# Optimization experiments

Hardware: AMD Instinct MI355X
Metric: run time of the kernel (lower is better)

The kernel has to match this reference:

```python
import jax, jax.numpy as jnp
import numpy as np

D_MODEL = 1024
NUM_HEADS = 16
D_K = D_MODEL // NUM_HEADS


def setup_inputs() -> dict:
    key = jax.random.key(0)
    ks = jax.random.split(key, 11)
    B, S = 2, 2048
    s = 1.0 / np.sqrt(D_MODEL)
    return {
        "query": jax.random.normal(ks[0], (B, S, D_MODEL), jnp.float32),
        "key": jax.random.normal(ks[1], (B, S, D_MODEL), jnp.float32),
        "value": jax.random.normal(ks[2], (B, S, D_MODEL), jnp.float32),
        "Wq": jax.random.normal(ks[3], (D_MODEL, D_MODEL), jnp.float32) * s,
        "bq": jnp.zeros((D_MODEL,), jnp.float32),
        "Wk": jax.random.normal(ks[4], (D_MODEL, D_MODEL), jnp.float32) * s,
        "bk": jnp.zeros((D_MODEL,), jnp.float32),
        "Wv": jax.random.normal(ks[5], (D_MODEL, D_MODEL), jnp.float32) * s,
        "bv": jnp.zeros((D_MODEL,), jnp.float32),
        "Wo": jax.random.normal(ks[6], (D_MODEL, D_MODEL), jnp.float32) * s,
        "bo": jnp.zeros((D_MODEL,), jnp.float32),
    }


def _split_heads(x):
    # [B, S, D] -> [B, H, S, d_k]
    B, S, _ = x.shape
    return x.reshape(B, S, NUM_HEADS, D_K).transpose(0, 2, 1, 3)


def reference(query, key, value, Wq, bq, Wk, bk, Wv, bv, Wo, bo):
    B, S, _ = query.shape
    q = _split_heads(query @ Wq + bq)   # [B, H, S, d_k]
    k = _split_heads(key @ Wk + bk)
    v = _split_heads(value @ Wv + bv)
    scores = jnp.einsum("bhqd,bhkd->bhqk", q, k) / jnp.sqrt(jnp.float32(D_K))
    attention_weights = jax.nn.softmax(scores, axis=-1)  # [B, H, S, S]
    context = jnp.einsum("bhqk,bhkd->bhqd", attention_weights, v)
    context = context.transpose(0, 2, 1, 3).reshape(B, S, D_MODEL)
    output = context @ Wo + bo
    return (output, attention_weights)
```

## Files before the change

kernel.cpp:

```cpp
#include <hip/hip_runtime.h>
#include <hip/hip_bf16.h>


#define SEQ   2048
#define DMODEL 1024
#define NH    16
#define DKH   64

typedef __attribute__((ext_vector_type(8))) short  short8;
typedef __attribute__((ext_vector_type(4))) float  floatx4;

__device__ __forceinline__ short f2bf(float f) {
    __hip_bfloat16 h = __float2bfloat16(f);
    return *reinterpret_cast<short*>(&h);
}
__device__ __forceinline__ unsigned int packbf(float a, float b) {
    return (unsigned int)(unsigned short)f2bf(a) | ((unsigned int)(unsigned short)f2bf(b) << 16);
}

__device__ __forceinline__ void gload_lds16(const short* g, short* l) {
    __builtin_amdgcn_global_load_lds(
        (const __attribute__((address_space(1))) void*)g,
        (__attribute__((address_space(3))) void*)l, 16, 0, 0);
}

__global__ void conv3(const float* __restrict__ s0, const float* __restrict__ s1,
                      const float* __restrict__ s2, short* __restrict__ d0,
                      short* __restrict__ d1, short* __restrict__ d2) {
    int z = blockIdx.z;
    const float* src = z == 0 ? s0 : z == 1 ? s1 : s2;
    short* dst       = z == 0 ? d0 : z == 1 ? d1 : d2;
    int i = blockIdx.x * blockDim.x + threadIdx.x;
    float4 v = reinterpret_cast<const float4*>(src)[i];
    short4 o;
    o.x = f2bf(v.x); o.y = f2bf(v.y); o.z = f2bf(v.z); o.w = f2bf(v.w);
    reinterpret_cast<short4*>(dst)[i] = o;
}

__global__ void conv_wt4(const float* __restrict__ W0, const float* __restrict__ W1,
                         const float* __restrict__ W2, const float* __restrict__ W3,
                         short* __restrict__ T0, short* __restrict__ T1,
                         short* __restrict__ T2, short* __restrict__ T3) {
    __shared__ short T[64 * 72];
    int z = blockIdx.z;
    const float* W = z == 0 ? W0 : z == 1 ? W1 : z == 2 ? W2 : W3;
    short* Wt      = z == 0 ? T0 : z == 1 ? T1 : z == 2 ? T2 : T3;
    int tid = threadIdx.x;
    int bk = blockIdx.y, bn = blockIdx.x;
    for (int i = 0; i < 4; i++) {
        int ch = i * 256 + tid;
        int r = ch >> 4, c4 = (ch & 15) * 4;
        float4 v = *(const float4*)&W[(size_t)(bk * 64 + r) * 1024 + bn * 64 + c4];
        T[(c4 + 0) * 72 + r] = f2bf(v.x);
        T[(c4 + 1) * 72 + r] = f2bf(v.y);
        T[(c4 + 2) * 72 + r] = f2bf(v.z);
        T[(c4 + 3) * 72 + r] = f2bf(v.w);
    }
    __syncthreads();
    for (int i = 0; i < 2; i++) {
        int ch = i * 256 + tid;
        int n = ch >> 3, k8 = (ch & 7) * 8;
        *(short8*)&Wt[(size_t)(bn * 64 + n) * 1024 + bk * 64 + k8] = *(const short8*)&T[n * 72 + k8];
    }
}

__device__ __forceinline__ void gemm_body(
    const short* __restrict__ A, const short* __restrict__ Bt,
    const float* __restrict__ bias, void* __restrict__ dst, int mode)
{
    __shared__ __align__(16) short As[2][128 * 32];
    __shared__ __align__(16) short Bs[2][64 * 32];
    int tid = threadIdx.x;
    int wave = tid >> 6, lane = tid & 63, quad = lane >> 4, l15 = lane & 15;
    int bm = blockIdx.y, bn = blockIdx.x;

    floatx4 acc[2][4];
#pragma unroll
    for (int i = 0; i < 2; i++)
#pragma unroll
        for (int j = 0; j < 4; j++) acc[i][j] = (floatx4){0.f, 0.f, 0.f, 0.f};

    const short* aBase = &A [(size_t)(bm * 128 + (tid >> 2)) * 1024 + (tid & 3) * 8];
    const short* bBase = &Bt[(size_t)(bn * 64  + (tid >> 2)) * 1024 + (tid & 3) * 8];

#define STAGE(buf, kb) do {                                              \
        gload_lds16(aBase + (kb) * 32,             &As[buf][(wave * 64) * 8]);         \
        gload_lds16(aBase + 64 * 1024 + (kb) * 32, &As[buf][(256 + wave * 64) * 8]);   \
        gload_lds16(bBase + (kb) * 32,             &Bs[buf][(wave * 64) * 8]);         \
    } while (0)

    STAGE(0, 0);
    __syncthreads();
    int cur = 0;
    for (int kb = 0; kb < 32; kb++) {
        if (kb < 31) STAGE(cur ^ 1, kb + 1);
        short8 ar[2], br[4];
#pragma unroll
        for (int mt = 0; mt < 2; mt++) ar[mt] = *(const short8*)&As[cur][(wave * 32 + mt * 16 + l15) * 32 + quad * 8];
#pragma unroll
        for (int nt = 0; nt < 4; nt++) br[nt] = *(const short8*)&Bs[cur][(nt * 16 + l15) * 32 + quad * 8];
#pragma unroll
        for (int mt = 0; mt < 2; mt++)
#pragma unroll
            for (int nt = 0; nt < 4; nt++)
                acc[mt][nt] = __builtin_amdgcn_mfma_f32_16x16x32_bf16(ar[mt], br[nt], acc[mt][nt], 0, 0, 0);
        __syncthreads();
        cur ^= 1;
    }
#undef STAGE

#pragma unroll
    for (int mt = 0; mt < 2; mt++) {
#pragma unroll
        for (int nt = 0; nt < 4; nt++) {
            int col = bn * 64 + nt * 16 + l15;
            float bb = bias[col];
#pragma unroll
            for (int r = 0; r < 4; r++) {
                int row = bm * 128 + wave * 32 + mt * 16 + quad * 4 + r;
                float v = acc[mt][nt][r] + bb;
                if (mode == 3) {
                    ((float*)dst)[(size_t)row * 1024 + col] = v;
                } else {
                    int b = row >> 11, s = row & 2047, h = col >> 6, dk = col & 63;
                    size_t idx;
                    if (mode == 0) idx = ((size_t)(b * NH + h) * SEQ + s) * DKH + dk;
                    else           idx = ((size_t)(b * NH + h) * DKH + dk) * SEQ + s;
                    ((short*)dst)[idx] = f2bf(v);
                }
            }
        }
    }
}

__global__ __launch_bounds__(256, 4) void gemm_qkv(
    const short* __restrict__ xq, const short* __restrict__ xk, const short* __restrict__ xv,
    const short* __restrict__ wq, const short* __restrict__ wk, const short* __restrict__ wv,
    const float* __restrict__ bq, const float* __restrict__ bk, const float* __restrict__ bv,
    short* __restrict__ qh, short* __restrict__ kh, short* __restrict__ vth)
{
    int z = blockIdx.z;
    const short* A  = z == 0 ? xq : z == 1 ? xk : xv;
    const short* Bt = z == 0 ? wq : z == 1 ? wk : wv;
    const float* bi = z == 0 ? bq : z == 1 ? bk : bv;
    short* dst      = z == 0 ? qh : z == 1 ? kh : vth;
    gemm_body(A, Bt, bi, dst, z == 2 ? 2 : 0);
}

__global__ __launch_bounds__(256, 4) void gemm_fin(
    const short* __restrict__ A, const short* __restrict__ Bt,
    const float* __restrict__ bias, float* __restrict__ dst)
{
    gemm_body(A, Bt, bias, dst, 3);
}

__global__ __launch_bounds__(256, 2) void attn_p1(
    const short* __restrict__ Q,
    const short* __restrict__ K,
    const short* __restrict__ Vt,
    float* __restrict__ rws,
    short* __restrict__ ctx)
{
    __shared__ __align__(16) short Qs [64 * 72];
    __shared__ __align__(16) short Ks [128 * 72];
    __shared__ __align__(16) short Vts[64 * 136];
    __shared__ __align__(16) short Ps [64 * 136];
    __shared__ float partial[4][64];
    __shared__ float rinv[64];

    int tid = threadIdx.x, wave = tid >> 6, lane = tid & 63, quad = lane >> 4, l15 = lane & 15;
    int qt = blockIdx.x, bh = blockIdx.y;
    int b = bh >> 4, h = bh & 15;
    const short* qb  = Q  + ((size_t)bh * SEQ + qt * 64) * DKH;
    const short* kbp = K  + (size_t)bh * SEQ * DKH;
    const short* vtb = Vt + (size_t)bh * DKH * SEQ;

#pragma unroll
    for (int c = 0; c < 2; c++) {
        int ch = tid * 2 + c; int row = ch >> 3, d = (ch & 7) * 8;
        *(short8*)&Qs[row * 72 + d] = *(const short8*)&qb[row * 64 + d];
    }

    short8 kreg[4], vreg[4];
#define LOADKV(kb) do {                                                              \
        _Pragma("unroll")                                                            \
        for (int c = 0; c < 4; c++) { int ch = tid * 4 + c; int row = ch >> 3, d = (ch & 7) * 8; \
            kreg[c] = *(const short8*)&kbp[(size_t)((kb) * 128 + row) * 64 + d]; }   \
        _Pragma("unroll")                                                            \
        for (int c = 0; c < 4; c++) { int ch = tid * 4 + c; int dd = ch >> 4, kq = (ch & 15) * 8; \
            vreg[c] = *(const short8*)&vtb[(size_t)dd * SEQ + (kb) * 128 + kq]; }    \
    } while (0)

    LOADKV(0);

    float rs[4][4];
#pragma unroll
    for (int i = 0; i < 4; i++)
#pragma unroll
        for (int r = 0; r < 4; r++) rs[i][r] = 0.f;
    floatx4 cacc[4];
#pragma unroll
    for (int i = 0; i < 4; i++) cacc[i] = (floatx4){0.f, 0.f, 0.f, 0.f};
    int nbase = wave * 32;

    for (int kb = 0; kb < SEQ / 128; kb++) {
        __syncthreads();
#pragma unroll
        for (int c = 0; c < 4; c++) {
            int ch = tid * 4 + c; int row = ch >> 3, d = (ch & 7) * 8;
            *(short8*)&Ks[row * 72 + d] = kreg[c];
        }
#pragma unroll
        for (int c = 0; c < 4; c++) {
            int ch = tid * 4 + c; int dd = ch >> 4, kq = (ch & 15) * 8;
            *(short8*)&Vts[dd * 136 + kq] = vreg[c];
        }
        __syncthreads();
        if (kb < SEQ / 128 - 1) LOADKV(kb + 1);

        floatx4 sacc[4][2];
#pragma unroll
        for (int mt = 0; mt < 4; mt++)
#pragma unroll
            for (int nt = 0; nt < 2; nt++) sacc[mt][nt] = (floatx4){0.f, 0.f, 0.f, 0.f};
#pragma unroll
        for (int kt = 0; kt < 2; kt++) {
            short8 ar[4], br[2];
#pragma unroll
            for (int mt = 0; mt < 4; mt++) ar[mt] = *(const short8*)&Qs[(mt * 16 + l15) * 72 + kt * 32 + quad * 8];
#pragma unroll
            for (int nt = 0; nt < 2; nt++) br[nt] = *(const short8*)&Ks[(nbase + 2 * l15 + nt) * 72 + kt * 32 + quad * 8];
#pragma unroll
            for (int mt = 0; mt < 4; mt++)
#pragma unroll
                for (int nt = 0; nt < 2; nt++)
                    sacc[mt][nt] = __builtin_amdgcn_mfma_f32_16x16x32_bf16(ar[mt], br[nt], sacc[mt][nt], 0, 0, 0);
        }
#pragma unroll
        for (int mt = 0; mt < 4; mt++) {
#pragma unroll
            for (int r = 0; r < 4; r++) {
                float e0 = __expf(sacc[mt][0][r] * 0.125f);
                float e1 = __expf(sacc[mt][1][r] * 0.125f);
                int row = mt * 16 + quad * 4 + r;
                *(unsigned int*)&Ps[row * 136 + nbase + 2 * l15] = packbf(e0, e1);
                rs[mt][r] += e0 + e1;
            }
        }
        __syncthreads();
#pragma unroll
        for (int kt = 0; kt < 4; kt++) {
            short8 pa = *(const short8*)&Ps[(wave * 16 + l15) * 136 + kt * 32 + quad * 8];
#pragma unroll
            for (int nt = 0; nt < 4; nt++) {
                short8 vb = *(const short8*)&Vts[(nt * 16 + l15) * 136 + kt * 32 + quad * 8];
                cacc[nt] = __builtin_amdgcn_mfma_f32_16x16x32_bf16(pa, vb, cacc[nt], 0, 0, 0);
            }
        }
    }
#undef LOADKV

#pragma unroll
    for (int mt = 0; mt < 4; mt++) {
#pragma unroll
        for (int r = 0; r < 4; r++) {
            float s = rs[mt][r];
            s += __shfl_xor(s, 1, 64); s += __shfl_xor(s, 2, 64);
            s += __shfl_xor(s, 4, 64); s += __shfl_xor(s, 8, 64);
            if (l15 == 0) partial[wave][mt * 16 + quad * 4 + r] = s;
        }
    }
    __syncthreads();
    if (tid < 64) {
        float ri = 1.f / (partial[0][tid] + partial[1][tid] + partial[2][tid] + partial[3][tid]);
        rinv[tid] = ri;
        rws[((size_t)bh * 32 + qt) * 64 + tid] = ri;
    }
    __syncthreads();

#pragma unroll
    for (int nt = 0; nt < 4; nt++) {
#pragma unroll
        for (int r = 0; r < 4; r++) {
            int row = wave * 16 + quad * 4 + r;
            int qg = qt * 64 + row;
            float v = cacc[nt][r] * rinv[row];
            ctx[((size_t)(b * SEQ + qg)) * DMODEL + h * DKH + nt * 16 + l15] = f2bf(v);
        }
    }
}

__global__ __launch_bounds__(256, 4) void attn_p2(
    const short* __restrict__ Q, const short* __restrict__ K,
    const float* __restrict__ rws, float* __restrict__ wout)
{
    __shared__ __align__(16) short Qs[64 * 72];
    __shared__ __align__(16) short Ks[128 * 72];
    __shared__ float rinv[64];

    int tid = threadIdx.x, wave = tid >> 6, lane = tid & 63, quad = lane >> 4, l15 = lane & 15;
    int qt = blockIdx.x, bh = blockIdx.y;
    const short* qb  = Q + ((size_t)bh * SEQ + qt * 64) * DKH;
    const short* kbp = K + (size_t)bh * SEQ * DKH;

#pragma unroll
    for (int c = 0; c < 2; c++) {
        int ch = tid * 2 + c; int row = ch >> 3, d = (ch & 7) * 8;
        *(short8*)&Qs[row * 72 + d] = *(const short8*)&qb[row * 64 + d];
    }
    if (tid < 64) rinv[tid] = rws[((size_t)bh * 32 + qt) * 64 + tid];

    short8 kreg[4];
#define LOADK(kb) do {                                                               \
        _Pragma("unroll")                                                            \
        for (int c = 0; c < 4; c++) { int ch = tid * 4 + c; int row = ch >> 3, d = (ch & 7) * 8; \
            kreg[c] = *(const short8*)&kbp[(size_t)((kb) * 128 + row) * 64 + d]; }   \
    } while (0)

    LOADK(0);
    int nbase = wave * 32;
    float* wb = wout + ((size_t)bh * SEQ + qt * 64) * SEQ;

    for (int kb = 0; kb < SEQ / 128; kb++) {
        __syncthreads();
#pragma unroll
        for (int c = 0; c < 4; c++) {
            int ch = tid * 4 + c; int row = ch >> 3, d = (ch & 7) * 8;
            *(short8*)&Ks[row * 72 + d] = kreg[c];
        }
        __syncthreads();
        if (kb < SEQ / 128 - 1) LOADK(kb + 1);

        floatx4 sacc[4][2];
#pragma unroll
        for (int mt = 0; mt < 4; mt++)
#pragma unroll
            for (int nt = 0; nt < 2; nt++) sacc[mt][nt] = (floatx4){0.f, 0.f, 0.f, 0.f};
#pragma unroll
        for (int kt = 0; kt < 2; kt++) {
            short8 ar[4], br[2];
#pragma unroll
            for (int mt = 0; mt < 4; mt++) ar[mt] = *(const short8*)&Qs[(mt * 16 + l15) * 72 + kt * 32 + quad * 8];
#pragma unroll
            for (int nt = 0; nt < 2; nt++) br[nt] = *(const short8*)&Ks[(nbase + 2 * l15 + nt) * 72 + kt * 32 + quad * 8];
#pragma unroll
            for (int mt = 0; mt < 4; mt++)
#pragma unroll
                for (int nt = 0; nt < 2; nt++)
                    sacc[mt][nt] = __builtin_amdgcn_mfma_f32_16x16x32_bf16(ar[mt], br[nt], sacc[mt][nt], 0, 0, 0);
        }
#pragma unroll
        for (int mt = 0; mt < 4; mt++) {
#pragma unroll
            for (int r = 0; r < 4; r++) {
                int row = mt * 16 + quad * 4 + r;
                float ri = rinv[row];
                float2 w2;
                w2.x = __expf(sacc[mt][0][r] * 0.125f) * ri;
                w2.y = __expf(sacc[mt][1][r] * 0.125f) * ri;
                *(float2*)&wb[(size_t)row * SEQ + kb * 128 + nbase + 2 * l15] = w2;
            }
        }
    }
#undef LOADK
}

extern "C" void kernel_launch(void* const* d_in, const int* in_sizes, int n_in,
                              void* d_out, int out_size, void* d_ws, size_t ws_size,
                              hipStream_t stream) {
    const float* query = (const float*)d_in[0];
    const float* key_  = (const float*)d_in[1];
    const float* value = (const float*)d_in[2];
    const float* Wq = (const float*)d_in[3];  const float* bq = (const float*)d_in[4];
    const float* Wk = (const float*)d_in[5];  const float* bk = (const float*)d_in[6];
    const float* Wv = (const float*)d_in[7];  const float* bv = (const float*)d_in[8];
    const float* Wo = (const float*)d_in[9];  const float* bo = (const float*)d_in[10];

    char* ws = (char*)d_ws;
    const size_t MB = 1ull << 20;
    short* xq  = (short*)(ws +  0 * MB);
    short* xk  = (short*)(ws +  8 * MB);
    short* xv  = (short*)(ws + 16 * MB);
    short* wtq = (short*)(ws + 24 * MB);
    short* wtk = (short*)(ws + 26 * MB);
    short* wtv = (short*)(ws + 28 * MB);
    short* wto = (short*)(ws + 30 * MB);
    short* qh  = (short*)(ws + 32 * MB);
    short* kh  = (short*)(ws + 40 * MB);
    short* vth = (short*)(ws + 48 * MB);
    short* ctx = (short*)(ws + 56 * MB);
    float* rws = (float*)(ws +  0 * MB);

    float* out0 = (float*)d_out;
    float* wout = out0 + (size_t)4194304;

    conv3<<<dim3(4096, 1, 3), 256, 0, stream>>>(query, key_, value, xq, xk, xv);
    conv_wt4<<<dim3(16, 16, 4), 256, 0, stream>>>(Wq, Wk, Wv, Wo, wtq, wtk, wtv, wto);

    gemm_qkv<<<dim3(16, 32, 3), 256, 0, stream>>>(xq, xk, xv, wtq, wtk, wtv,
                                                  bq, bk, bv, qh, kh, vth);

    attn_p1<<<dim3(SEQ / 64, 32), 256, 0, stream>>>(qh, kh, vth, rws, ctx);
    attn_p2<<<dim3(SEQ / 64, 32), 256, 0, stream>>>(qh, kh, rws, wout);

    gemm_fin<<<dim3(16, 32), 256, 0, stream>>>(ctx, wto, bo, out0);
}
```

Measured before the change: 759.5 us.

## Split key range across waves in attention pass one with register-resident fragments

The first attention pass now has each wave own a disjoint slice of keys. It uses 32x32x16 MFMAs with Q, K and V^T fragments loaded straight from global memory into registers. The probability tile is rebuilt in registers with lane shuffles instead of going through LDS. Per-wave context partials are reduced through a shared float slab at the end. The second pass also keeps Q fragments in registers and reads K directly from global memory, dropping the LDS staging and per-iteration barriers. The aim is to remove LDS traffic and synchronisation, at the cost of uncoalesced or redundant global loads and higher register pressure.

Result: no change. 768.4 us (+1.2%).

```diff
diff --git a/kernel.cpp b/kernel.cpp
--- a/kernel.cpp
+++ b/kernel.cpp
@@ -7,8 +7,9 @@
 #define NH    16
 #define DKH   64
 
-typedef __attribute__((ext_vector_type(8))) short  short8;
-typedef __attribute__((ext_vector_type(4))) float  floatx4;
+typedef __attribute__((ext_vector_type(8)))  short short8;
+typedef __attribute__((ext_vector_type(4)))  float floatx4;
+typedef __attribute__((ext_vector_type(16))) float floatx16;
 
 __device__ __forceinline__ short f2bf(float f) {
     __hip_bfloat16 h = __float2bfloat16(f);
@@ -83,7 +84,7 @@
     const short* aBase = &A [(size_t)(bm * 128 + (tid >> 2)) * 1024 + (tid & 3) * 8];
     const short* bBase = &Bt[(size_t)(bn * 64  + (tid >> 2)) * 1024 + (tid & 3) * 8];
 
-#define STAGE(buf, kb) do {                                              \
+#define STAGE(buf, kb) do {                                                            \
         gload_lds16(aBase + (kb) * 32,             &As[buf][(wave * 64) * 8]);         \
         gload_lds16(aBase + 64 * 1024 + (kb) * 32, &As[buf][(256 + wave * 64) * 8]);   \
         gload_lds16(bBase + (kb) * 32,             &Bs[buf][(wave * 64) * 8]);         \
@@ -161,141 +162,137 @@
     float* __restrict__ rws,
     short* __restrict__ ctx)
 {
-    __shared__ __align__(16) short Qs [64 * 72];
-    __shared__ __align__(16) short Ks [128 * 72];
-    __shared__ __align__(16) short Vts[64 * 136];
-    __shared__ __align__(16) short Ps [64 * 136];
+    __shared__ float Cs[4][64 * 68];
     __shared__ float partial[4][64];
-    __shared__ float rinv[64];
-
-    int tid = threadIdx.x, wave = tid >> 6, lane = tid & 63, quad = lane >> 4, l15 = lane & 15;
+
+    int tid = threadIdx.x, wave = tid >> 6, lane = tid & 63;
+    int l31 = lane & 31, hh2 = lane >> 5;
     int qt = blockIdx.x, bh = blockIdx.y;
-    int b = bh >> 4, h = bh & 15;
-    const short* qb  = Q  + ((size_t)bh * SEQ + qt * 64) * DKH;
-    const short* kbp = K  + (size_t)bh * SEQ * DKH;
-    const short* vtb = Vt + (size_t)bh * DKH * SEQ;
-
-#pragma unroll
-    for (int c = 0; c < 2; c++) {
-        int ch = tid * 2 + c; int row = ch >> 3, d = (ch & 7) * 8;
-        *(short8*)&Qs[row * 72 + d] = *(const short8*)&qb[row * 64 + d];
-    }
-
-    short8 kreg[4], vreg[4];
-#define LOADKV(kb) do {                                                              \
-        _Pragma("unroll")                                                            \
-        for (int c = 0; c < 4; c++) { int ch = tid * 4 + c; int row = ch >> 3, d = (ch & 7) * 8; \
-            kreg[c] = *(const short8*)&kbp[(size_t)((kb) * 128 + row) * 64 + d]; }   \
-        _Pragma("unroll")                                                            \
-        for (int c = 0; c < 4; c++) { int ch = tid * 4 + c; int dd = ch >> 4, kq = (ch & 15) * 8; \
-            vreg[c] = *(const short8*)&vtb[(size_t)dd * SEQ + (kb) * 128 + kq]; }    \
-    } while (0)
-
-    LOADKV(0);
-
-    float rs[4][4];
-#pragma unroll
-    for (int i = 0; i < 4; i++)
-#pragma unroll
-        for (int r = 0; r < 4; r++) rs[i][r] = 0.f;
-    floatx4 cacc[4];
-#pragma unroll
-    for (int i = 0; i < 4; i++) cacc[i] = (floatx4){0.f, 0.f, 0.f, 0.f};
-    int nbase = wave * 32;
-
-    for (int kb = 0; kb < SEQ / 128; kb++) {
-        __syncthreads();
-#pragma unroll
-        for (int c = 0; c < 4; c++) {
-            int ch = tid * 4 + c; int row = ch >> 3, d = (ch & 7) * 8;
-            *(short8*)&Ks[row * 72 + d] = kreg[c];
+    int b = bh >> 4, hd = bh & 15;
+
+    const short* qb = Q  + ((size_t)bh * SEQ + qt * 64) * DKH;
+    const short* kb = K  + (size_t)bh * SEQ * DKH;
+    const short* vb = Vt + (size_t)bh * DKH * SEQ;
+
+    short8 qf[2][4];
+#pragma unroll
+    for (int nt = 0; nt < 2; nt++)
+#pragma unroll
+        for (int kt = 0; kt < 4; kt++)
+            qf[nt][kt] = *(const short8*)&qb[(nt * 32 + l31) * 64 + kt * 16 + hh2 * 8];
+
+    floatx16 cacc[2][2];
+#pragma unroll
+    for (int i = 0; i < 2; i++)
+#pragma unroll
+        for (int j = 0; j < 2; j++)
+#pragma unroll
+            for (int r = 0; r < 16; r++) cacc[i][j][r] = 0.f;
+    float rs[2] = {0.f, 0.f};
+
+    for (int kbase = wave * 32; kbase < SEQ; kbase += 128) {
+        short8 kf[4];
+#pragma unroll
+        for (int kt = 0; kt < 4; kt++)
+            kf[kt] = *(const short8*)&kb[(size_t)(kbase + l31) * 64 + kt * 16 + hh2 * 8];
+        short8 vf[2][2];
+#pragma unroll
+        for (int nt = 0; nt < 2; nt++)
+#pragma unroll
+            for (int s = 0; s < 2; s++)
+                vf[nt][s] = *(const short8*)&vb[(size_t)(nt * 32 + l31) * SEQ + kbase + s * 16 + hh2 * 8];
+
+        floatx16 sacc[2];
+#pragma unroll
+        for (int nt = 0; nt < 2; nt++)
+#pragma unroll
+            for (int r = 0; r < 16; r++) sacc[nt][r] = 0.f;
+#pragma unroll
+        for (int kt = 0; kt < 4; kt++)
+#pragma unroll
+            for (int nt = 0; nt < 2; nt++)
+                sacc[nt] = __builtin_amdgcn_mfma_f32_32x32x16_bf16(kf[kt], qf[nt][kt], sacc[nt], 0, 0, 0);
+
+        short8 pfrag[2][2];
+#pragma unroll
+        for (int nt = 0; nt < 2; nt++) {
+            float e[16];
+            float sum = 0.f;
+#pragma unroll
+            for (int r = 0; r < 16; r++) {
+                e[r] = __expf(sacc[nt][r] * 0.125f);
+                sum += e[r];
+            }
+            rs[nt] += sum;
+            unsigned int pk[8], X[8];
+#pragma unroll
+            for (int j = 0; j < 8; j++) pk[j] = packbf(e[2 * j], e[2 * j + 1]);
+#pragma unroll
+            for (int j = 0; j < 8; j++) X[j] = __shfl_xor(pk[j], 32, 64);
+#pragma unroll
+            for (int s = 0; s < 2; s++) {
+                unsigned int u[4];
+                u[0] = hh2 ? X[4 * s + 2]  : pk[4 * s + 0];
+                u[1] = hh2 ? X[4 * s + 3]  : pk[4 * s + 1];
+                u[2] = hh2 ? pk[4 * s + 2] : X[4 * s + 0];
+                u[3] = hh2 ? pk[4 * s + 3] : X[4 * s + 1];
+                pfrag[nt][s] = *reinterpret_cast<short8*>(u);
+            }
         }
-#pragma unroll
-        for (int c = 0; c < 4; c++) {
-            int ch = tid * 4 + c; int dd = ch >> 4, kq = (ch & 15) * 8;
-            *(short8*)&Vts[dd * 136 + kq] = vreg[c];
-        }
-        __syncthreads();
-        if (kb < SEQ / 128 - 1) LOADKV(kb + 1);
-
-        floatx4 sacc[4][2];
-#pragma unroll
-        for (int mt = 0; mt < 4; mt++)
-#pragma unroll
-            for (int nt = 0; nt < 2; nt++) sacc[mt][nt] = (floatx4){0.f, 0.f, 0.f, 0.f};
-#pragma unroll
-        for (int kt = 0; kt < 2; kt++) {
-            short8 ar[4], br[2];
-#pragma unroll
-            for (int mt = 0; mt < 4; mt++) ar[mt] = *(const short8*)&Qs[(mt * 16 + l15) * 72 + kt * 32 + quad * 8];
-#pragma unroll
-            for (int nt = 0; nt < 2; nt++) br[nt] = *(const short8*)&Ks[(nbase + 2 * l15 + nt) * 72 + kt * 32 + quad * 8];
-#pragma unroll
-            for (int mt = 0; mt < 4; mt++)
+
+#pragma unroll
+        for (int s = 0; s < 2; s++)
+#pragma unroll
+            for (int mt = 0; mt < 2; mt++)
 #pragma unroll
                 for (int nt = 0; nt < 2; nt++)
-                    sacc[mt][nt] = __builtin_amdgcn_mfma_f32_16x16x32_bf16(ar[mt], br[nt], sacc[mt][nt], 0, 0, 0);
-        }
-#pragma unroll
-        for (int mt = 0; mt < 4; mt++) {
-#pragma unroll
-            for (int r = 0; r < 4; r++) {
-                float e0 = __expf(sacc[mt][0][r] * 0.125f);
-                float e1 = __expf(sacc[mt][1][r] * 0.125f);
-                int row = mt * 16 + quad * 4 + r;
-                *(unsigned int*)&Ps[row * 136 + nbase + 2 * l15] = packbf(e0, e1);
-                rs[mt][r] += e0 + e1;
-            }
-        }
-        __syncthreads();
-#pragma unroll
-        for (int kt = 0; kt < 4; kt++) {
-            short8 pa = *(const short8*)&Ps[(wave * 16 + l15) * 136 + kt * 32 + quad * 8];
-#pragma unroll
-            for (int nt = 0; nt < 4; nt++) {
-                short8 vb = *(const short8*)&Vts[(nt * 16 + l15) * 136 + kt * 32 + quad * 8];
-                cacc[nt] = __builtin_amdgcn_mfma_f32_16x16x32_bf16(pa, vb, cacc[nt], 0, 0, 0);
-            }
-        }
-    }
-#undef LOADKV
-
-#pragma unroll
-    for (int mt = 0; mt < 4; mt++) {
-#pragma unroll
-        for (int r = 0; r < 4; r++) {
-            float s = rs[mt][r];
-            s += __shfl_xor(s, 1, 64); s += __shfl_xor(s, 2, 64);
-            s += __shfl_xor(s, 4, 64); s += __shfl_xor(s, 8, 64);
-            if (l15 == 0) partial[wave][mt * 16 + quad * 4 + r] = s;
-        }
-    }
+                    cacc[mt][nt] = __builtin_amdgcn_mfma_f32_32x32x16_bf16(pfrag[mt][s], vf[nt][s], cacc[mt][nt], 0, 0, 0);
+    }
+
+    rs[0] += __shfl_xor(rs[0], 32, 64);
+    rs[1] += __shfl_xor(rs[1], 32, 64);
+    if (hh2 == 0) {
+        partial[wave][l31]      = rs[0];
+        partial[wave][32 + l31] = rs[1];
+    }
+    float* slab = &Cs[wave][0];
+#pragma unroll
+    for (int mt = 0; mt < 2; mt++)
+#pragma unroll
+        for (int nt = 0; nt < 2; nt++)
+#pragma unroll
+            for (int r = 0; r < 16; r++) {
+                int q = mt * 32 + (r & 3) + 8 * (r >> 2) + 4 * hh2;
+                int d = nt * 32 + l31;
+                slab[q * 68 + d] = cacc[mt][nt][r];
+            }
     __syncthreads();
-    if (tid < 64) {
-        float ri = 1.f / (partial[0][tid] + partial[1][tid] + partial[2][tid] + partial[3][tid]);
-        rinv[tid] = ri;
-        rws[((size_t)bh * 32 + qt) * 64 + tid] = ri;
-    }
-    __syncthreads();
-
-#pragma unroll
-    for (int nt = 0; nt < 4; nt++) {
-#pragma unroll
-        for (int r = 0; r < 4; r++) {
-            int row = wave * 16 + quad * 4 + r;
-            int qg = qt * 64 + row;
-            float v = cacc[nt][r] * rinv[row];
-            ctx[((size_t)(b * SEQ + qg)) * DMODEL + h * DKH + nt * 16 + l15] = f2bf(v);
-        }
-    }
+
+    int q = tid >> 2, d0 = (tid & 3) * 16;
+    float rinvv = 1.f / (partial[0][q] + partial[1][q] + partial[2][q] + partial[3][q]);
+    if ((tid & 3) == 0) rws[((size_t)bh * 32 + qt) * 64 + q] = rinvv;
+
+    short ov[16];
+#pragma unroll
+    for (int c = 0; c < 4; c++) {
+        float4 a = *(const float4*)&Cs[0][q * 68 + d0 + c * 4];
+        float4 x1 = *(const float4*)&Cs[1][q * 68 + d0 + c * 4];
+        float4 x2 = *(const float4*)&Cs[2][q * 68 + d0 + c * 4];
+        float4 x3 = *(const float4*)&Cs[3][q * 68 + d0 + c * 4];
+        ov[c * 4 + 0] = f2bf((a.x + x1.x + x2.x + x3.x) * rinvv);
+        ov[c * 4 + 1] = f2bf((a.y + x1.y + x2.y + x3.y) * rinvv);
+        ov[c * 4 + 2] = f2bf((a.z + x1.z + x2.z + x3.z) * rinvv);
+        ov[c * 4 + 3] = f2bf((a.w + x1.w + x2.w + x3.w) * rinvv);
+    }
+    size_t row = (size_t)(b * SEQ + qt * 64 + q);
+    *(short8*)&ctx[row * DMODEL + hd * DKH + d0]     = *(short8*)&ov[0];
+    *(short8*)&ctx[row * DMODEL + hd * DKH + d0 + 8] = *(short8*)&ov[8];
 }
 
 __global__ __launch_bounds__(256, 4) void attn_p2(
     const short* __restrict__ Q, const short* __restrict__ K,
     const float* __restrict__ rws, float* __restrict__ wout)
 {
-    __shared__ __align__(16) short Qs[64 * 72];
-    __shared__ __align__(16) short Ks[128 * 72];
     __shared__ float rinv[64];
 
     int tid = threadIdx.x, wave = tid >> 6, lane = tid & 63, quad = lane >> 4, l15 = lane & 15;
@@ -303,33 +300,26 @@
     const short* qb  = Q + ((size_t)bh * SEQ + qt * 64) * DKH;
     const short* kbp = K + (size_t)bh * SEQ * DKH;
 
-#pragma unroll
-    for (int c = 0; c < 2; c++) {
-        int ch = tid * 2 + c; int row = ch >> 3, d = (ch & 7) * 8;
-        *(short8*)&Qs[row * 72 + d] = *(const short8*)&qb[row * 64 + d];
-    }
     if (tid < 64) rinv[tid] = rws[((size_t)bh * 32 + qt) * 64 + tid];
 
-    short8 kreg[4];
-#define LOADK(kb) do {                                                               \
-        _Pragma("unroll")                                                            \
-        for (int c = 0; c < 4; c++) { int ch = tid * 4 + c; int row = ch >> 3, d = (ch & 7) * 8; \
-            kreg[c] = *(const short8*)&kbp[(size_t)((kb) * 128 + row) * 64 + d]; }   \
-    } while (0)
-
-    LOADK(0);
+    short8 qf[4][2];
+#pragma unroll
+    for (int mt = 0; mt < 4; mt++)
+#pragma unroll
+        for (int kt = 0; kt < 2; kt++)
+            qf[mt][kt] = *(const short8*)&qb[(mt * 16 + l15) * 64 + kt * 32 + quad * 8];
+    __syncthreads();
+
     int nbase = wave * 32;
     float* wb = wout + ((size_t)bh * SEQ + qt * 64) * SEQ;
 
     for (int kb = 0; kb < SEQ / 128; kb++) {
-        __syncthreads();
-#pragma unroll
-        for (int c = 0; c < 4; c++) {
-            int ch = tid * 4 + c; int row = ch >> 3, d = (ch & 7) * 8;
-            *(short8*)&Ks[row * 72 + d] = kreg[c];
-        }
-        __syncthreads();
-        if (kb < SEQ / 128 - 1) LOADK(kb + 1);
+        short8 bf[2][2];
+#pragma unroll
+        for (int nt = 0; nt < 2; nt++)
+#pragma unroll
+            for (int kt = 0; kt < 2; kt++)
+                bf[nt][kt] = *(const short8*)&kbp[(size_t)(kb * 128 + nbase + 2 * l15 + nt) * 64 + kt * 32 + quad * 8];
 
         floatx4 sacc[4][2];
 #pragma unroll
@@ -337,18 +327,12 @@
 #pragma unroll
             for (int nt = 0; nt < 2; nt++) sacc[mt][nt] = (floatx4){0.f, 0.f, 0.f, 0.f};
 #pragma unroll
-        for (int kt = 0; kt < 2; kt++) {
-            short8 ar[4], br[2];
-#pragma unroll
-            for (int mt = 0; mt < 4; mt++) ar[mt] = *(const short8*)&Qs[(mt * 16 + l15) * 72 + kt * 32 + quad * 8];
-#pragma unroll
-            for (int nt = 0; nt < 2; nt++) br[nt] = *(const short8*)&Ks[(nbase + 2 * l15 + nt) * 72 + kt * 32 + quad * 8];
+        for (int kt = 0; kt < 2; kt++)
 #pragma unroll
             for (int mt = 0; mt < 4; mt++)
 #pragma unroll
                 for (int nt = 0; nt < 2; nt++)
-                    sacc[mt][nt] = __builtin_amdgcn_mfma_f32_16x16x32_bf16(ar[mt], br[nt], sacc[mt][nt], 0, 0, 0);
-        }
+                    sacc[mt][nt] = __builtin_amdgcn_mfma_f32_16x16x32_bf16(qf[mt][kt], bf[nt][kt], sacc[mt][nt], 0, 0, 0);
 #pragma unroll
         for (int mt = 0; mt < 4; mt++) {
 #pragma unroll
@@ -362,7 +346,6 @@
             }
         }
     }
-#undef LOADK
 }
 
 extern "C" void kernel_launch(void* const* d_in, const int* in_sizes, int n_in,
```
